# Kernel optimization log

Measured on AMD Instinct MI355X. Metric: run time of the kernel, lower is better.

The kernel has to match this reference:

```python
import jax, jax.numpy as jnp
import numpy as np

N_NODES = 100000
N_EDGES = 3200000
D_NODE = 32
D_EDGE = 6


def _mlp2(x, W1, b1, W2, b2):
    # Linear -> ReLU -> Linear -> ReLU
    h = jax.nn.relu(x @ W1 + b1)
    return jax.nn.relu(h @ W2 + b2)


def setup_inputs() -> dict:
    key = jax.random.key(0)
    ks = jax.random.split(key, 12)
    glorot = lambda k, fi, fo: jax.random.normal(k, (fi, fo), jnp.float32) * (2.0 / (fi + fo)) ** 0.5
    return {
        "x_node": jax.random.normal(ks[0], (N_NODES, D_NODE), jnp.float32),
        "x_edge": jax.random.normal(ks[1], (N_EDGES, D_EDGE), jnp.float32),
        "src": jax.random.randint(ks[2], (N_EDGES,), 0, N_NODES, jnp.int32),
        "dst": jax.random.randint(ks[3], (N_EDGES,), 0, N_NODES, jnp.int32),
        # edge_msg_encoder: 70 -> 32 -> 6
        "We1": glorot(ks[4], 70, 32), "be1": jnp.zeros((32,), jnp.float32),
        "We2": glorot(ks[5], 32, 6), "be2": jnp.zeros((6,), jnp.float32),
        # node_msg_encoder: 38 -> 64 -> 32
        "Wn1": glorot(ks[6], 38, 64), "bn1": jnp.zeros((64,), jnp.float32),
        "Wn2": glorot(ks[7], 64, 32), "bn2": jnp.zeros((32,), jnp.float32),
    }


def reference(x_node, x_edge, src, dst, We1, be1, We2, be2, Wn1, bn1, Wn2, bn2):
    # Gather endpoint node features per edge
    x_dst = x_node[dst]                                   # [E, 32]
    x_src = x_node[src]                                   # [E, 32]
    edge_in = jnp.concatenate([x_dst, x_src, x_edge], 1)  # [E, 70]
    edge_msg = _mlp2(edge_in, We1, be1, We2, be2)         # [E, 6]
    node_in = jnp.concatenate([x_dst, edge_msg], 1)       # [E, 38]
    node_msg = _mlp2(node_in, Wn1, bn1, Wn2, bn2)         # [E, 32]
    # reduce_udf: sum of incoming messages per destination node
    nm = jax.ops.segment_sum(node_msg, dst, num_segments=N_NODES)  # [N, 32]
    return nm, edge_msg
```

## Files before the change

kernel.cpp:

```cpp
#include <hip/hip_runtime.h>

#define N_EDGES 3200000
#define N_NODES 100000

typedef __attribute__((ext_vector_type(8))) short bf16x8;
typedef __attribute__((ext_vector_type(4))) float f32x4;

__device__ inline unsigned short f2bf(float f) {
    unsigned u = __float_as_uint(f);
    u += 0x7fffu + ((u >> 16) & 1u);
    return (unsigned short)(u >> 16);
}
__device__ inline unsigned pack_bf2(float lo, float hi) {
    return (unsigned)f2bf(lo) | ((unsigned)f2bf(hi) << 16);
}
__device__ inline float bflo(unsigned u) { return __uint_as_float(u << 16); }
__device__ inline float bfhi(unsigned u) { return __uint_as_float(u & 0xffff0000u); }

__global__ void __launch_bounds__(256) mpn_precompute(
    const float* __restrict__ x_node,
    const float* __restrict__ We1, const float* __restrict__ be1,
    const float* __restrict__ Wn1, const float* __restrict__ bn1,
    const float* __restrict__ Wn2,
    unsigned* __restrict__ Pd, unsigned* __restrict__ Ps,
    short* __restrict__ Wn2T,
    float* __restrict__ nm_out)
{
    const int n = blockIdx.x * 256 + threadIdx.x;
    if (n >= N_NODES) return;

    {
        float4 z = make_float4(0.f, 0.f, 0.f, 0.f);
        float4* o = (float4*)(nm_out + (size_t)n * 32);
        #pragma unroll
        for (int i = 0; i < 8; ++i) o[i] = z;
    }
    if (n < 2048) Wn2T[n] = (short)f2bf(Wn2[(n & 63) * 32 + (n >> 6)]);

    float x[32];
    {
        const float4* px = (const float4*)(x_node + (size_t)n * 32);
        #pragma unroll
        for (int i = 0; i < 8; ++i) {
            float4 v = px[i];
            x[4*i+0] = v.x; x[4*i+1] = v.y; x[4*i+2] = v.z; x[4*i+3] = v.w;
        }
    }

    float p1[32];
    #pragma unroll
    for (int j = 0; j < 32; ++j) p1[j] = be1[j];
    for (int k = 0; k < 32; ++k) {
        const float a = x[k];
        const float* w = We1 + k * 32;
        #pragma unroll
        for (int j = 0; j < 32; ++j) p1[j] = fmaf(a, w[j], p1[j]);
    }
    unsigned* pd = Pd + (size_t)n * 48;
    #pragma unroll
    for (int i = 0; i < 16; ++i) pd[i] = pack_bf2(p1[2*i], p1[2*i+1]);

    float p3[64];
    #pragma unroll
    for (int j = 0; j < 64; ++j) p3[j] = bn1[j];
    for (int k = 0; k < 32; ++k) {
        const float a = x[k];
        const float* w = Wn1 + k * 64;
        #pragma unroll
        for (int j = 0; j < 64; ++j) p3[j] = fmaf(a, w[j], p3[j]);
    }
    #pragma unroll
    for (int i = 0; i < 32; ++i) pd[16 + i] = pack_bf2(p3[2*i], p3[2*i+1]);

    float p2[32];
    #pragma unroll
    for (int j = 0; j < 32; ++j) p2[j] = 0.0f;
    for (int k = 0; k < 32; ++k) {
        const float a = x[k];
        const float* w = We1 + (32 + k) * 32;
        #pragma unroll
        for (int j = 0; j < 32; ++j) p2[j] = fmaf(a, w[j], p2[j]);
    }
    unsigned* ps = Ps + (size_t)n * 16;
    #pragma unroll
    for (int i = 0; i < 16; ++i) ps[i] = pack_bf2(p2[2*i], p2[2*i+1]);
}

__global__ void __launch_bounds__(256, 5) mpn_main(
    const unsigned* __restrict__ Pd,
    const unsigned* __restrict__ Ps,
    const float* __restrict__ x_edge,
    const int* __restrict__ src,
    const int* __restrict__ dst,
    const float* __restrict__ We1,
    const float* __restrict__ We2, const float* __restrict__ be2,
    const float* __restrict__ Wn1,
    const short* __restrict__ Wn2T,
    const float* __restrict__ bn2,
    float* __restrict__ nm_out,
    float* __restrict__ em_out)
{
    __shared__ alignas(16) unsigned smem[8192];

    const int tid  = threadIdx.x;
    const int lane = tid & 63;
    const int wave = tid >> 6;
    const int quad = lane >> 4;
    const int l15  = lane & 15;

    const int e = blockIdx.x * 256 + tid;
    const int d = dst[e];
    const int s = src[e];

    const uint4* pdrow = (const uint4*)(Pd + (size_t)d * 48);
    const uint4* psrow = (const uint4*)(Ps + (size_t)s * 16);

    float xe[6];
    {
        const float2* pe = (const float2*)(x_edge + (size_t)e * 6);
        float2 a = pe[0], b = pe[1], c = pe[2];
        xe[0]=a.x; xe[1]=a.y; xe[2]=b.x; xe[3]=b.y; xe[4]=c.x; xe[5]=c.y;
    }

    float h1[32];
    #pragma unroll
    for (int i = 0; i < 4; ++i) {
        uint4 va = pdrow[i];
        uint4 vb = psrow[i];
        h1[8*i+0] = bflo(va.x) + bflo(vb.x);
        h1[8*i+1] = bfhi(va.x) + bfhi(vb.x);
        h1[8*i+2] = bflo(va.y) + bflo(vb.y);
        h1[8*i+3] = bfhi(va.y) + bfhi(vb.y);
        h1[8*i+4] = bflo(va.z) + bflo(vb.z);
        h1[8*i+5] = bfhi(va.z) + bfhi(vb.z);
        h1[8*i+6] = bflo(va.w) + bflo(vb.w);
        h1[8*i+7] = bfhi(va.w) + bfhi(vb.w);
    }

    const uint4 q0 = pdrow[4],  q1 = pdrow[5],  q2 = pdrow[6],  q3 = pdrow[7];
    const uint4 q4 = pdrow[8],  q5 = pdrow[9],  q6 = pdrow[10], q7 = pdrow[11];

    #pragma unroll
    for (int k = 0; k < 6; ++k) {
        const float a = xe[k];
        const float* w = We1 + (64 + k) * 32;
        #pragma unroll
        for (int j = 0; j < 32; ++j) h1[j] = fmaf(a, w[j], h1[j]);
    }
    #pragma unroll
    for (int j = 0; j < 32; ++j) h1[j] = fmaxf(h1[j], 0.0f);

    float em[6];
    #pragma unroll
    for (int j = 0; j < 6; ++j) em[j] = be2[j];
    for (int k = 0; k < 32; ++k) {
        const float a = h1[k];
        const float* w = We2 + k * 6;
        #pragma unroll
        for (int j = 0; j < 6; ++j) em[j] = fmaf(a, w[j], em[j]);
    }
    #pragma unroll
    for (int j = 0; j < 6; ++j) em[j] = fmaxf(em[j], 0.0f);

    {
        float2* eo = (float2*)(em_out + (size_t)e * 6);
        eo[0] = make_float2(em[0], em[1]);
        eo[1] = make_float2(em[2], em[3]);
        eo[2] = make_float2(em[4], em[5]);
    }

    float h2[64];
    {
        uint4 qq[8] = {q0, q1, q2, q3, q4, q5, q6, q7};
        #pragma unroll
        for (int i = 0; i < 8; ++i) {
            uint4 v = qq[i];
            h2[8*i+0] = bflo(v.x); h2[8*i+1] = bfhi(v.x);
            h2[8*i+2] = bflo(v.y); h2[8*i+3] = bfhi(v.y);
            h2[8*i+4] = bflo(v.z); h2[8*i+5] = bfhi(v.z);
            h2[8*i+6] = bflo(v.w); h2[8*i+7] = bfhi(v.w);
        }
    }
    #pragma unroll
    for (int k = 0; k < 6; ++k) {
        const float a = em[k];
        const float* w = Wn1 + (32 + k) * 64;
        #pragma unroll
        for (int j = 0; j < 64; ++j) h2[j] = fmaf(a, w[j], h2[j]);
    }

    unsigned* tile = smem + wave * 2048;
    {
        char* tb = (char*)tile + lane * 128;
        const int sx = (lane & 7) << 4;
        #pragma unroll
        for (int i = 0; i < 8; ++i) {
            uint4 v;
            v.x = pack_bf2(fmaxf(h2[8*i+0],0.f), fmaxf(h2[8*i+1],0.f));
            v.y = pack_bf2(fmaxf(h2[8*i+2],0.f), fmaxf(h2[8*i+3],0.f));
            v.z = pack_bf2(fmaxf(h2[8*i+4],0.f), fmaxf(h2[8*i+5],0.f));
            v.w = pack_bf2(fmaxf(h2[8*i+6],0.f), fmaxf(h2[8*i+7],0.f));
            *(uint4*)(tb + ((i * 16) ^ sx)) = v;
        }
    }

    bf16x8 bfr[2][2];
    #pragma unroll
    for (int n = 0; n < 2; ++n)
        #pragma unroll
        for (int kt = 0; kt < 2; ++kt)
            bfr[n][kt] = *(const bf16x8*)(Wn2T + (n*16 + l15)*64 + kt*32 + quad*8);

    f32x4 acc[4][2];
    #pragma unroll
    for (int m = 0; m < 4; ++m) { acc[m][0] = (f32x4)0.f; acc[m][1] = (f32x4)0.f; }

    #pragma unroll
    for (int m = 0; m < 4; ++m) {
        const int R = m * 16 + l15;
        const char* ar = (const char*)tile + R * 128;
        const int rx = (R & 7) << 4;
        #pragma unroll
        for (int kt = 0; kt < 2; ++kt) {
            bf16x8 af = *(const bf16x8*)(ar + ((kt*64 + quad*16) ^ rx));
            acc[m][0] = __builtin_amdgcn_mfma_f32_16x16x32_bf16(af, bfr[0][kt], acc[m][0], 0, 0, 0);
            acc[m][1] = __builtin_amdgcn_mfma_f32_16x16x32_bf16(af, bfr[1][kt], acc[m][1], 0, 0, 0);
        }
    }
    __syncthreads();

    unsigned* s_nmb = smem;
    int*      s_d   = (int*)(smem + 4096);
    s_d[tid] = d;

    const float b0 = bn2[l15];
    const float b1 = bn2[16 + l15];
    #pragma unroll
    for (int m = 0; m < 4; ++m)
        #pragma unroll
        for (int r = 0; r < 4; ++r) {
            const int row = wave*64 + m*16 + quad*4 + r;
            s_nmb[row*16 + l15] =
                pack_bf2(fmaxf(acc[m][0][r] + b0, 0.f),
                         fmaxf(acc[m][1][r] + b1, 0.f));
        }
    __syncthreads();

    #pragma unroll 4
    for (int it = 0; it < 16; ++it) {
        const int idx = it * 256 + tid;
        const int row = idx >> 4;
        const int w   = idx & 15;
        const unsigned u = s_nmb[row*16 + w];
        float* base = nm_out + (size_t)s_d[row] * 32 + w;
        atomicAdd(base,      bflo(u));
        atomicAdd(base + 16, bfhi(u));
    }
}

extern "C" void kernel_launch(void* const* d_in, const int* in_sizes, int n_in,
                              void* d_out, int out_size, void* d_ws, size_t ws_size,
                              hipStream_t stream) {
    const float* x_node = (const float*)d_in[0];
    const float* x_edge = (const float*)d_in[1];
    const int*   src    = (const int*)d_in[2];
    const int*   dst    = (const int*)d_in[3];
    const float* We1 = (const float*)d_in[4];
    const float* be1 = (const float*)d_in[5];
    const float* We2 = (const float*)d_in[6];
    const float* be2 = (const float*)d_in[7];
    const float* Wn1 = (const float*)d_in[8];
    const float* bn1 = (const float*)d_in[9];
    const float* Wn2 = (const float*)d_in[10];
    const float* bn2 = (const float*)d_in[11];

    float* nm_out = (float*)d_out;
    float* em_out = (float*)d_out + (size_t)N_NODES * 32;

    unsigned* Pd   = (unsigned*)d_ws;
    unsigned* Ps   = Pd + (size_t)N_NODES * 48;
    short*    Wn2T = (short*)(Ps + (size_t)N_NODES * 16);

    mpn_precompute<<<(N_NODES + 255) / 256, 256, 0, stream>>>(
        x_node, We1, be1, Wn1, bn1, Wn2, Pd, Ps, Wn2T, nm_out);

    mpn_main<<<N_EDGES / 256, 256, 0, stream>>>(
        Pd, Ps, x_edge, src, dst,
        We1, We2, be2, Wn1, Wn2T, bn2,
        nm_out, em_out);
}
```

Before: 555.4 us.

## Move per-edge MLP layers onto MFMA and gather raw bf16 node features

The per-node precompute of layer-1 partial products is replaced by storing bf16 copies of x_node plus transposed bf16 weight tiles, with the biases folded in through a constant-one input column. The main kernel then runs every edge and node MLP layer as 16x16x32 bf16 MFMAs, using edges as the N dimension, and moves activations between layers with wave shuffles instead of shared-memory tiles. Each block now handles 128 edges and launch bounds drop to 4 waves per EU. This cuts the per-edge gather from 256 B to 128 B and removes the scalar FMA loops, at the cost of more MFMA and shuffle work and bf16 rounding of inputs and the edge_msg path.

```diff
diff --git a/kernel.cpp b/kernel.cpp
--- a/kernel.cpp
+++ b/kernel.cpp
@@ -3,6 +3,7 @@
 #define N_EDGES 3200000
 #define N_NODES 100000
 
+typedef unsigned short ushort_t;
 typedef __attribute__((ext_vector_type(8))) short bf16x8;
 typedef __attribute__((ext_vector_type(4))) float f32x4;
 
@@ -16,17 +17,45 @@
 }
 __device__ inline float bflo(unsigned u) { return __uint_as_float(u << 16); }
 __device__ inline float bfhi(unsigned u) { return __uint_as_float(u & 0xffff0000u); }
+__device__ inline bf16x8 u4_to_b8(uint4 u) {
+    union { uint4 a; bf16x8 b; } c; c.a = u; return c.b;
+}
 
 __global__ void __launch_bounds__(256) mpn_precompute(
     const float* __restrict__ x_node,
     const float* __restrict__ We1, const float* __restrict__ be1,
+    const float* __restrict__ We2, const float* __restrict__ be2,
     const float* __restrict__ Wn1, const float* __restrict__ bn1,
     const float* __restrict__ Wn2,
-    unsigned* __restrict__ Pd, unsigned* __restrict__ Ps,
-    short* __restrict__ Wn2T,
+    unsigned* __restrict__ xb,
+    ushort_t* __restrict__ WaT, ushort_t* __restrict__ WbT,
+    ushort_t* __restrict__ WcTp, ushort_t* __restrict__ W2T,
+    ushort_t* __restrict__ NaT, ushort_t* __restrict__ NbTp,
+    ushort_t* __restrict__ N2T, float* __restrict__ be2p,
     float* __restrict__ nm_out)
 {
     const int n = blockIdx.x * 256 + threadIdx.x;
+
+    if (n < 1024) {
+        const int o = n >> 5, k = n & 31;
+        WaT[n] = f2bf(We1[k * 32 + o]);
+        WbT[n] = f2bf(We1[(32 + k) * 32 + o]);
+        WcTp[n] = (k < 6) ? f2bf(We1[(64 + k) * 32 + o])
+                          : ((k == 6) ? f2bf(be1[o]) : (ushort_t)0);
+    }
+    if (n < 512) {
+        const int o = n >> 5, k = n & 31;
+        W2T[n] = (o < 6) ? f2bf(We2[k * 6 + o]) : (ushort_t)0;
+    }
+    if (n < 2048) {
+        const int o = n >> 5, k = n & 31;
+        NaT[n] = f2bf(Wn1[k * 64 + o]);
+        NbTp[n] = (k < 6) ? f2bf(Wn1[(32 + k) * 64 + o])
+                          : ((k == 6) ? f2bf(bn1[o]) : (ushort_t)0);
+        N2T[n] = f2bf(Wn2[(n & 63) * 32 + (n >> 6)]);
+    }
+    if (n < 16) be2p[n] = (n < 6) ? be2[n] : 0.0f;
+
     if (n >= N_NODES) return;
 
     {
@@ -35,223 +64,185 @@
         #pragma unroll
         for (int i = 0; i < 8; ++i) o[i] = z;
     }
-    if (n < 2048) Wn2T[n] = (short)f2bf(Wn2[(n & 63) * 32 + (n >> 6)]);
-
-    float x[32];
     {
         const float4* px = (const float4*)(x_node + (size_t)n * 32);
+        unsigned* xr = xb + (size_t)n * 16;
         #pragma unroll
         for (int i = 0; i < 8; ++i) {
             float4 v = px[i];
-            x[4*i+0] = v.x; x[4*i+1] = v.y; x[4*i+2] = v.z; x[4*i+3] = v.w;
-        }
-    }
-
-    float p1[32];
-    #pragma unroll
-    for (int j = 0; j < 32; ++j) p1[j] = be1[j];
-    for (int k = 0; k < 32; ++k) {
-        const float a = x[k];
-        const float* w = We1 + k * 32;
-        #pragma unroll
-        for (int j = 0; j < 32; ++j) p1[j] = fmaf(a, w[j], p1[j]);
-    }
-    unsigned* pd = Pd + (size_t)n * 48;
-    #pragma unroll
-    for (int i = 0; i < 16; ++i) pd[i] = pack_bf2(p1[2*i], p1[2*i+1]);
-
-    float p3[64];
-    #pragma unroll
-    for (int j = 0; j < 64; ++j) p3[j] = bn1[j];
-    for (int k = 0; k < 32; ++k) {
-        const float a = x[k];
-        const float* w = Wn1 + k * 64;
-        #pragma unroll
-        for (int j = 0; j < 64; ++j) p3[j] = fmaf(a, w[j], p3[j]);
-    }
-    #pragma unroll
-    for (int i = 0; i < 32; ++i) pd[16 + i] = pack_bf2(p3[2*i], p3[2*i+1]);
-
-    float p2[32];
-    #pragma unroll
-    for (int j = 0; j < 32; ++j) p2[j] = 0.0f;
-    for (int k = 0; k < 32; ++k) {
-        const float a = x[k];
-        const float* w = We1 + (32 + k) * 32;
-        #pragma unroll
-        for (int j = 0; j < 32; ++j) p2[j] = fmaf(a, w[j], p2[j]);
-    }
-    unsigned* ps = Ps + (size_t)n * 16;
-    #pragma unroll
-    for (int i = 0; i < 16; ++i) ps[i] = pack_bf2(p2[2*i], p2[2*i+1]);
-}
-
-__global__ void __launch_bounds__(256, 5) mpn_main(
-    const unsigned* __restrict__ Pd,
-    const unsigned* __restrict__ Ps,
+            xr[2*i+0] = pack_bf2(v.x, v.y);
+            xr[2*i+1] = pack_bf2(v.z, v.w);
+        }
+    }
+}
+
+__global__ void __launch_bounds__(256, 4) mpn_main(
+    const ushort_t* __restrict__ xb,
+    const ushort_t* __restrict__ WaT, const ushort_t* __restrict__ WbT,
+    const ushort_t* __restrict__ WcTp, const ushort_t* __restrict__ W2T,
+    const ushort_t* __restrict__ NaT, const ushort_t* __restrict__ NbTp,
+    const ushort_t* __restrict__ N2T,
+    const float* __restrict__ be2p, const float* __restrict__ bn2,
     const float* __restrict__ x_edge,
-    const int* __restrict__ src,
-    const int* __restrict__ dst,
-    const float* __restrict__ We1,
-    const float* __restrict__ We2, const float* __restrict__ be2,
-    const float* __restrict__ Wn1,
-    const short* __restrict__ Wn2T,
-    const float* __restrict__ bn2,
+    const int* __restrict__ src, const int* __restrict__ dst,
     float* __restrict__ nm_out,
     float* __restrict__ em_out)
 {
-    __shared__ alignas(16) unsigned smem[8192];
+    __shared__ unsigned s_nmb[128 * 17];
+    __shared__ int s_d[128];
 
     const int tid  = threadIdx.x;
     const int lane = tid & 63;
     const int wave = tid >> 6;
-    const int quad = lane >> 4;
+    const int q    = (lane >> 4) & 3;
     const int l15  = lane & 15;
-
-    const int e = blockIdx.x * 256 + tid;
-    const int d = dst[e];
-    const int s = src[e];
-
-    const uint4* pdrow = (const uint4*)(Pd + (size_t)d * 48);
-    const uint4* psrow = (const uint4*)(Ps + (size_t)s * 16);
-
-    float xe[6];
-    {
-        const float2* pe = (const float2*)(x_edge + (size_t)e * 6);
-        float2 a = pe[0], b = pe[1], c = pe[2];
-        xe[0]=a.x; xe[1]=a.y; xe[2]=b.x; xe[3]=b.y; xe[4]=c.x; xe[5]=c.y;
-    }
-
-    float h1[32];
-    #pragma unroll
-    for (int i = 0; i < 4; ++i) {
-        uint4 va = pdrow[i];
-        uint4 vb = psrow[i];
-        h1[8*i+0] = bflo(va.x) + bflo(vb.x);
-        h1[8*i+1] = bfhi(va.x) + bfhi(vb.x);
-        h1[8*i+2] = bflo(va.y) + bflo(vb.y);
-        h1[8*i+3] = bfhi(va.y) + bfhi(vb.y);
-        h1[8*i+4] = bflo(va.z) + bflo(vb.z);
-        h1[8*i+5] = bfhi(va.z) + bfhi(vb.z);
-        h1[8*i+6] = bflo(va.w) + bflo(vb.w);
-        h1[8*i+7] = bfhi(va.w) + bfhi(vb.w);
-    }
-
-    const uint4 q0 = pdrow[4],  q1 = pdrow[5],  q2 = pdrow[6],  q3 = pdrow[7];
-    const uint4 q4 = pdrow[8],  q5 = pdrow[9],  q6 = pdrow[10], q7 = pdrow[11];
-
-    #pragma unroll
-    for (int k = 0; k < 6; ++k) {
-        const float a = xe[k];
-        const float* w = We1 + (64 + k) * 32;
-        #pragma unroll
-        for (int j = 0; j < 32; ++j) h1[j] = fmaf(a, w[j], h1[j]);
-    }
-    #pragma unroll
-    for (int j = 0; j < 32; ++j) h1[j] = fmaxf(h1[j], 0.0f);
-
-    float em[6];
-    #pragma unroll
-    for (int j = 0; j < 6; ++j) em[j] = be2[j];
-    for (int k = 0; k < 32; ++k) {
-        const float a = h1[k];
-        const float* w = We2 + k * 6;
-        #pragma unroll
-        for (int j = 0; j < 6; ++j) em[j] = fmaf(a, w[j], em[j]);
-    }
-    #pragma unroll
-    for (int j = 0; j < 6; ++j) em[j] = fmaxf(em[j], 0.0f);
-
-    {
-        float2* eo = (float2*)(em_out + (size_t)e * 6);
-        eo[0] = make_float2(em[0], em[1]);
-        eo[1] = make_float2(em[2], em[3]);
-        eo[2] = make_float2(em[4], em[5]);
-    }
-
-    float h2[64];
-    {
-        uint4 qq[8] = {q0, q1, q2, q3, q4, q5, q6, q7};
-        #pragma unroll
-        for (int i = 0; i < 8; ++i) {
-            uint4 v = qq[i];
-            h2[8*i+0] = bflo(v.x); h2[8*i+1] = bfhi(v.x);
-            h2[8*i+2] = bflo(v.y); h2[8*i+3] = bfhi(v.y);
-            h2[8*i+4] = bflo(v.z); h2[8*i+5] = bfhi(v.z);
-            h2[8*i+6] = bflo(v.w); h2[8*i+7] = bfhi(v.w);
-        }
-    }
-    #pragma unroll
-    for (int k = 0; k < 6; ++k) {
-        const float a = em[k];
-        const float* w = Wn1 + (32 + k) * 64;
-        #pragma unroll
-        for (int j = 0; j < 64; ++j) h2[j] = fmaf(a, w[j], h2[j]);
-    }
-
-    unsigned* tile = smem + wave * 2048;
-    {
-        char* tb = (char*)tile + lane * 128;
-        const int sx = (lane & 7) << 4;
-        #pragma unroll
-        for (int i = 0; i < 8; ++i) {
-            uint4 v;
-            v.x = pack_bf2(fmaxf(h2[8*i+0],0.f), fmaxf(h2[8*i+1],0.f));
-            v.y = pack_bf2(fmaxf(h2[8*i+2],0.f), fmaxf(h2[8*i+3],0.f));
-            v.z = pack_bf2(fmaxf(h2[8*i+4],0.f), fmaxf(h2[8*i+5],0.f));
-            v.w = pack_bf2(fmaxf(h2[8*i+6],0.f), fmaxf(h2[8*i+7],0.f));
-            *(uint4*)(tb + ((i * 16) ^ sx)) = v;
-        }
-    }
-
-    bf16x8 bfr[2][2];
-    #pragma unroll
-    for (int n = 0; n < 2; ++n)
-        #pragma unroll
-        for (int kt = 0; kt < 2; ++kt)
-            bfr[n][kt] = *(const bf16x8*)(Wn2T + (n*16 + l15)*64 + kt*32 + quad*8);
-
-    f32x4 acc[4][2];
-    #pragma unroll
-    for (int m = 0; m < 4; ++m) { acc[m][0] = (f32x4)0.f; acc[m][1] = (f32x4)0.f; }
-
-    #pragma unroll
-    for (int m = 0; m < 4; ++m) {
-        const int R = m * 16 + l15;
-        const char* ar = (const char*)tile + R * 128;
-        const int rx = (R & 7) << 4;
-        #pragma unroll
-        for (int kt = 0; kt < 2; ++kt) {
-            bf16x8 af = *(const bf16x8*)(ar + ((kt*64 + quad*16) ^ rx));
-            acc[m][0] = __builtin_amdgcn_mfma_f32_16x16x32_bf16(af, bfr[0][kt], acc[m][0], 0, 0, 0);
-            acc[m][1] = __builtin_amdgcn_mfma_f32_16x16x32_bf16(af, bfr[1][kt], acc[m][1], 0, 0, 0);
-        }
+    const int hi   = q >> 1;
+
+    const int eb = blockIdx.x * 128 + wave * 32;
+
+    int dv[2], sv[2];
+    #pragma unroll
+    for (int t = 0; t < 2; ++t) {
+        const int e = eb + t * 16 + l15;
+        dv[t] = dst[e];
+        sv[t] = src[e];
+    }
+    bf16x8 xd[2], xs[2];
+    #pragma unroll
+    for (int t = 0; t < 2; ++t) {
+        xd[t] = *(const bf16x8*)(xb + (size_t)dv[t] * 32 + q * 8);
+        xs[t] = *(const bf16x8*)(xb + (size_t)sv[t] * 32 + q * 8);
+    }
+    uint4 bxeU[2];
+    #pragma unroll
+    for (int t = 0; t < 2; ++t) {
+        uint4 u = make_uint4(0, 0, 0, 0);
+        if (q == 0) {
+            const int e = eb + t * 16 + l15;
+            const float2* pe = (const float2*)(x_edge + (size_t)e * 6);
+            float2 a = pe[0], b = pe[1], c = pe[2];
+            u = make_uint4(pack_bf2(a.x, a.y), pack_bf2(b.x, b.y),
+                           pack_bf2(c.x, c.y), pack_bf2(1.0f, 0.0f));
+        }
+        bxeU[t] = u;
+    }
+
+    const int sAl = ((q & 1) << 5) + l15;
+    const int sBl = sAl + 16;
+
+    #pragma unroll
+    for (int t = 0; t < 2; ++t) {
+        f32x4 h1c[2];
+        #pragma unroll
+        for (int m = 0; m < 2; ++m) {
+            const int row = m * 16 + l15;
+            f32x4 acc = (f32x4)0.f;
+            acc = __builtin_amdgcn_mfma_f32_16x16x32_bf16(
+                *(const bf16x8*)(WaT + row * 32 + q * 8), xd[t], acc, 0, 0, 0);
+            acc = __builtin_amdgcn_mfma_f32_16x16x32_bf16(
+                *(const bf16x8*)(WbT + row * 32 + q * 8), xs[t], acc, 0, 0, 0);
+            acc = __builtin_amdgcn_mfma_f32_16x16x32_bf16(
+                *(const bf16x8*)(WcTp + row * 32 + q * 8), u4_to_b8(bxeU[t]), acc, 0, 0, 0);
+            #pragma unroll
+            for (int r = 0; r < 4; ++r) acc[r] = fmaxf(acc[r], 0.f);
+            h1c[m] = acc;
+        }
+
+        unsigned u00 = pack_bf2(h1c[0][0], h1c[0][1]);
+        unsigned u01 = pack_bf2(h1c[0][2], h1c[0][3]);
+        unsigned u10 = pack_bf2(h1c[1][0], h1c[1][1]);
+        unsigned u11 = pack_bf2(h1c[1][2], h1c[1][3]);
+        unsigned a0 = __shfl((int)u00, sAl), a1 = __shfl((int)u01, sAl);
+        unsigned a2 = __shfl((int)u10, sAl), a3 = __shfl((int)u11, sAl);
+        unsigned b0 = __shfl((int)u00, sBl), b1 = __shfl((int)u01, sBl);
+        unsigned b2 = __shfl((int)u10, sBl), b3 = __shfl((int)u11, sBl);
+        uint4 bh1 = make_uint4(hi ? a2 : a0, hi ? a3 : a1,
+                               hi ? b2 : b0, hi ? b3 : b1);
+
+        f32x4 emc = __builtin_amdgcn_mfma_f32_16x16x32_bf16(
+            *(const bf16x8*)(W2T + l15 * 32 + q * 8), u4_to_b8(bh1),
+            (f32x4)0.f, 0, 0, 0);
+        const float emv0 = fmaxf(emc[0] + be2p[q * 4 + 0], 0.f);
+        const float emv1 = fmaxf(emc[1] + be2p[q * 4 + 1], 0.f);
+        const float emv2 = fmaxf(emc[2] + be2p[q * 4 + 2], 0.f);
+        const float emv3 = fmaxf(emc[3] + be2p[q * 4 + 3], 0.f);
+
+        const int e = eb + t * 16 + l15;
+        if (q == 0) {
+            *(float2*)(em_out + (size_t)e * 6 + 0) = make_float2(emv0, emv1);
+            *(float2*)(em_out + (size_t)e * 6 + 2) = make_float2(emv2, emv3);
+        } else if (q == 1) {
+            *(float2*)(em_out + (size_t)e * 6 + 4) = make_float2(emv0, emv1);
+        }
+
+        const float f4 = __shfl(emv0, l15 + 16);
+        const float f5 = __shfl(emv1, l15 + 16);
+        uint4 bem = make_uint4(0, 0, 0, 0);
+        if (q == 0)
+            bem = make_uint4(pack_bf2(emv0, emv1), pack_bf2(emv2, emv3),
+                             pack_bf2(f4, f5), pack_bf2(1.0f, 0.0f));
+
+        f32x4 h2c[4];
+        #pragma unroll
+        for (int m = 0; m < 4; ++m) {
+            const int row = m * 16 + l15;
+            f32x4 acc = __builtin_amdgcn_mfma_f32_16x16x32_bf16(
+                *(const bf16x8*)(NbTp + row * 32 + q * 8), u4_to_b8(bem),
+                (f32x4)0.f, 0, 0, 0);
+            acc = __builtin_amdgcn_mfma_f32_16x16x32_bf16(
+                *(const bf16x8*)(NaT + row * 32 + q * 8), xd[t], acc, 0, 0, 0);
+            #pragma unroll
+            for (int r = 0; r < 4; ++r) acc[r] = fmaxf(acc[r], 0.f);
+            h2c[m] = acc;
+        }
+
+        unsigned v00 = pack_bf2(h2c[0][0], h2c[0][1]), v01 = pack_bf2(h2c[0][2], h2c[0][3]);
+        unsigned v10 = pack_bf2(h2c[1][0], h2c[1][1]), v11 = pack_bf2(h2c[1][2], h2c[1][3]);
+        unsigned v20 = pack_bf2(h2c[2][0], h2c[2][1]), v21 = pack_bf2(h2c[2][2], h2c[2][3]);
+        unsigned v30 = pack_bf2(h2c[3][0], h2c[3][1]), v31 = pack_bf2(h2c[3][2], h2c[3][3]);
+        unsigned c0 = __shfl((int)v00, sAl), c1 = __shfl((int)v01, sAl);
+        unsigned c2 = __shfl((int)v10, sAl), c3 = __shfl((int)v11, sAl);
+        unsigned d0 = __shfl((int)v00, sBl), d1 = __shfl((int)v01, sBl);
+        unsigned d2 = __shfl((int)v10, sBl), d3 = __shfl((int)v11, sBl);
+        uint4 bh2k0 = make_uint4(hi ? c2 : c0, hi ? c3 : c1,
+                                 hi ? d2 : d0, hi ? d3 : d1);
+        unsigned g0 = __shfl((int)v20, sAl), g1 = __shfl((int)v21, sAl);
+        unsigned g2 = __shfl((int)v30, sAl), g3 = __shfl((int)v31, sAl);
+        unsigned k0 = __shfl((int)v20, sBl), k1 = __shfl((int)v21, sBl);
+        unsigned k2 = __shfl((int)v30, sBl), k3 = __shfl((int)v31, sBl);
+        uint4 bh2k1 = make_uint4(hi ? g2 : g0, hi ? g3 : g1,
+                                 hi ? k2 : k0, hi ? k3 : k1);
+
+        f32x4 nm0 = __builtin_amdgcn_mfma_f32_16x16x32_bf16(
+            *(const bf16x8*)(N2T + (0 * 16 + l15) * 64 + q * 8), u4_to_b8(bh2k0),
+            (f32x4)0.f, 0, 0, 0);
+        nm0 = __builtin_amdgcn_mfma_f32_16x16x32_bf16(
+            *(const bf16x8*)(N2T + (0 * 16 + l15) * 64 + 32 + q * 8), u4_to_b8(bh2k1),
+            nm0, 0, 0, 0);
+        f32x4 nm1 = __builtin_amdgcn_mfma_f32_16x16x32_bf16(
+            *(const bf16x8*)(N2T + (1 * 16 + l15) * 64 + q * 8), u4_to_b8(bh2k0),
+            (f32x4)0.f, 0, 0, 0);
+        nm1 = __builtin_amdgcn_mfma_f32_16x16x32_bf16(
+            *(const bf16x8*)(N2T + (1 * 16 + l15) * 64 + 32 + q * 8), u4_to_b8(bh2k1),
+            nm1, 0, 0, 0);
+
+        #pragma unroll
+        for (int r = 0; r < 4; ++r) {
+            const int f = q * 4 + r;
+            s_nmb[(wave * 32 + t * 16 + l15) * 17 + f] =
+                pack_bf2(fmaxf(nm0[r] + bn2[f], 0.f),
+                         fmaxf(nm1[r] + bn2[16 + f], 0.f));
+        }
+        if (q == 0) s_d[wave * 32 + t * 16 + l15] = dv[t];
     }
     __syncthreads();
 
-    unsigned* s_nmb = smem;
-    int*      s_d   = (int*)(smem + 4096);
-    s_d[tid] = d;
-
-    const float b0 = bn2[l15];
-    const float b1 = bn2[16 + l15];
-    #pragma unroll
-    for (int m = 0; m < 4; ++m)
-        #pragma unroll
-        for (int r = 0; r < 4; ++r) {
-            const int row = wave*64 + m*16 + quad*4 + r;
-            s_nmb[row*16 + l15] =
-                pack_bf2(fmaxf(acc[m][0][r] + b0, 0.f),
-                         fmaxf(acc[m][1][r] + b1, 0.f));
-        }
-    __syncthreads();
-
     #pragma unroll 4
-    for (int it = 0; it < 16; ++it) {
+    for (int it = 0; it < 8; ++it) {
         const int idx = it * 256 + tid;
         const int row = idx >> 4;
         const int w   = idx & 15;
-        const unsigned u = s_nmb[row*16 + w];
+        const unsigned u = s_nmb[row * 17 + w];
         float* base = nm_out + (size_t)s_d[row] * 32 + w;
         atomicAdd(base,      bflo(u));
         atomicAdd(base + 16, bfhi(u));
@@ -277,15 +268,22 @@
     float* nm_out = (float*)d_out;
     float* em_out = (float*)d_out + (size_t)N_NODES * 32;
 
-    unsigned* Pd   = (unsigned*)d_ws;
-    unsigned* Ps   = Pd + (size_t)N_NODES * 48;
-    short*    Wn2T = (short*)(Ps + (size_t)N_NODES * 16);
+    char* ws = (char*)d_ws;
+    unsigned* xb    = (unsigned*)ws;
+    ushort_t* WaT   = (ushort_t*)(ws + 6400000);
+    ushort_t* WbT   = (ushort_t*)(ws + 6402048);
+    ushort_t* WcTp  = (ushort_t*)(ws + 6404096);
+    ushort_t* W2T   = (ushort_t*)(ws + 6406144);
+    ushort_t* NaT   = (ushort_t*)(ws + 6407168);
+    ushort_t* NbTp  = (ushort_t*)(ws + 6411264);
+    ushort_t* N2T   = (ushort_t*)(ws + 6415360);
+    float*    be2p  = (float*)(ws + 6419456);
 
     mpn_precompute<<<(N_NODES + 255) / 256, 256, 0, stream>>>(
-        x_node, We1, be1, Wn1, bn1, Wn2, Pd, Ps, Wn2T, nm_out);
-
-    mpn_main<<<N_EDGES / 256, 256, 0, stream>>>(
-        Pd, Ps, x_edge, src, dst,
-        We1, We2, be2, Wn1, Wn2T, bn2,
-        nm_out, em_out);
-}
+        x_node, We1, be1, We2, be2, Wn1, bn1, Wn2,
+        xb, WaT, WbT, WcTp, W2T, NaT, NbTp, N2T, be2p, nm_out);
+
+    mpn_main<<<N_EDGES / 128, 256, 0, stream>>>(
+        (const ushort_t*)xb, WaT, WbT, WcTp, W2T, NaT, NbTp, N2T,
+        be2p, bn2, x_edge, src, dst, nm_out, em_out);
+}
```

After: 551.3 us. No clear change (-0.7%).

## Use padded LDS tiles and chunked fp32 scatter in edge kernel

Applied to the files above, without the earlier changes.

Replaces the XOR-swizzled LDS tile with a row-padded [64][36] layout for the MFMA A operand. The scatter stage now stages fp32 node messages in two 128-edge chunks with a 33-float padded stride, so atomics add full-precision values instead of bf16-packed ones. It also drops the occupancy hint from the launch bounds and moves the x_edge load later. The trade is one extra barrier round per chunk and possibly different LDS usage and occupancy.

```diff
diff --git a/kernel.cpp b/kernel.cpp
--- a/kernel.cpp
+++ b/kernel.cpp
@@ -86,7 +86,7 @@
     for (int i = 0; i < 16; ++i) ps[i] = pack_bf2(p2[2*i], p2[2*i+1]);
 }
 
-__global__ void __launch_bounds__(256, 5) mpn_main(
+__global__ void __launch_bounds__(256) mpn_main(
     const unsigned* __restrict__ Pd,
     const unsigned* __restrict__ Ps,
     const float* __restrict__ x_edge,
@@ -100,7 +100,8 @@
     float* __restrict__ nm_out,
     float* __restrict__ em_out)
 {
-    __shared__ alignas(16) unsigned smem[8192];
+    __shared__ unsigned s_h2[4][64][36];
+    __shared__ int      s_dst[128];
 
     const int tid  = threadIdx.x;
     const int lane = tid & 63;
@@ -114,13 +115,6 @@
 
     const uint4* pdrow = (const uint4*)(Pd + (size_t)d * 48);
     const uint4* psrow = (const uint4*)(Ps + (size_t)s * 16);
-
-    float xe[6];
-    {
-        const float2* pe = (const float2*)(x_edge + (size_t)e * 6);
-        float2 a = pe[0], b = pe[1], c = pe[2];
-        xe[0]=a.x; xe[1]=a.y; xe[2]=b.x; xe[3]=b.y; xe[4]=c.x; xe[5]=c.y;
-    }
 
     float h1[32];
     #pragma unroll
@@ -140,6 +134,12 @@
     const uint4 q0 = pdrow[4],  q1 = pdrow[5],  q2 = pdrow[6],  q3 = pdrow[7];
     const uint4 q4 = pdrow[8],  q5 = pdrow[9],  q6 = pdrow[10], q7 = pdrow[11];
 
+    float xe[6];
+    {
+        const float2* pe = (const float2*)(x_edge + (size_t)e * 6);
+        float2 a = pe[0], b = pe[1], c = pe[2];
+        xe[0]=a.x; xe[1]=a.y; xe[2]=b.x; xe[3]=b.y; xe[4]=c.x; xe[5]=c.y;
+    }
     #pragma unroll
     for (int k = 0; k < 6; ++k) {
         const float a = xe[k];
@@ -189,10 +189,8 @@
         for (int j = 0; j < 64; ++j) h2[j] = fmaf(a, w[j], h2[j]);
     }
 
-    unsigned* tile = smem + wave * 2048;
-    {
-        char* tb = (char*)tile + lane * 128;
-        const int sx = (lane & 7) << 4;
+    {
+        uint4* row = (uint4*)&s_h2[wave][lane][0];
         #pragma unroll
         for (int i = 0; i < 8; ++i) {
             uint4 v;
@@ -200,7 +198,7 @@
             v.y = pack_bf2(fmaxf(h2[8*i+2],0.f), fmaxf(h2[8*i+3],0.f));
             v.z = pack_bf2(fmaxf(h2[8*i+4],0.f), fmaxf(h2[8*i+5],0.f));
             v.w = pack_bf2(fmaxf(h2[8*i+6],0.f), fmaxf(h2[8*i+7],0.f));
-            *(uint4*)(tb + ((i * 16) ^ sx)) = v;
+            row[i] = v;
         }
     }
 
@@ -217,44 +215,47 @@
 
     #pragma unroll
     for (int m = 0; m < 4; ++m) {
-        const int R = m * 16 + l15;
-        const char* ar = (const char*)tile + R * 128;
-        const int rx = (R & 7) << 4;
         #pragma unroll
         for (int kt = 0; kt < 2; ++kt) {
-            bf16x8 af = *(const bf16x8*)(ar + ((kt*64 + quad*16) ^ rx));
+            bf16x8 af = *(const bf16x8*)((const char*)&s_h2[wave][m*16 + l15][0]
+                                         + kt*64 + quad*16);
             acc[m][0] = __builtin_amdgcn_mfma_f32_16x16x32_bf16(af, bfr[0][kt], acc[m][0], 0, 0, 0);
             acc[m][1] = __builtin_amdgcn_mfma_f32_16x16x32_bf16(af, bfr[1][kt], acc[m][1], 0, 0, 0);
         }
     }
-    __syncthreads();
-
-    unsigned* s_nmb = smem;
-    int*      s_d   = (int*)(smem + 4096);
-    s_d[tid] = d;
 
     const float b0 = bn2[l15];
     const float b1 = bn2[16 + l15];
-    #pragma unroll
-    for (int m = 0; m < 4; ++m)
-        #pragma unroll
-        for (int r = 0; r < 4; ++r) {
-            const int row = wave*64 + m*16 + quad*4 + r;
-            s_nmb[row*16 + l15] =
-                pack_bf2(fmaxf(acc[m][0][r] + b0, 0.f),
-                         fmaxf(acc[m][1][r] + b1, 0.f));
-        }
-    __syncthreads();
-
-    #pragma unroll 4
-    for (int it = 0; it < 16; ++it) {
-        const int idx = it * 256 + tid;
-        const int row = idx >> 4;
-        const int w   = idx & 15;
-        const unsigned u = s_nmb[row*16 + w];
-        float* base = nm_out + (size_t)s_d[row] * 32 + w;
-        atomicAdd(base,      bflo(u));
-        atomicAdd(base + 16, bfhi(u));
+
+    float* s_nm = (float*)s_h2;
+    #pragma unroll
+    for (int chunk = 0; chunk < 2; ++chunk) {
+        __syncthreads();
+        if ((tid >> 7) == chunk) {
+            s_dst[tid & 127] = d;
+            const int be = (wave & 1) * 64;
+            #pragma unroll
+            for (int m = 0; m < 4; ++m) {
+                #pragma unroll
+                for (int n = 0; n < 2; ++n) {
+                    const float bb = n ? b1 : b0;
+                    #pragma unroll
+                    for (int r = 0; r < 4; ++r) {
+                        const int le  = be + m*16 + quad*4 + r;
+                        const int out = n*16 + l15;
+                        s_nm[le*33 + out] = fmaxf(acc[m][n][r] + bb, 0.0f);
+                    }
+                }
+            }
+        }
+        __syncthreads();
+        #pragma unroll 4
+        for (int it = 0; it < 16; ++it) {
+            const int f  = it * 256 + tid;
+            const int le = f >> 5;
+            const int j  = f & 31;
+            atomicAdd(nm_out + (size_t)s_dst[le] * 32 + j, s_nm[le*33 + j]);
+        }
     }
 }
 
```

After: 550.4 us. Within noise of the previous version (-0.9%).
